# Performance work log

Hardware: AMD Instinct MI355X
Metric: run time of the kernel (lower is better)

The kernel has to match this reference:

```python
import jax, jax.numpy as jnp
import numpy as np
from jax import lax

THETA = 1.0      # neuron['theta']
TAU_SR = 10.0    # neuron['tauSr'] (SRM synaptic time constant)
TAU_RHO = 1.0    # surrogate-gradient width
SCALE_RHO = 1.0  # surrogate-gradient scale
T_SIM = 100      # simulation['tSample']


def srm_kernel(T, dtype=jnp.float32):
    t = jnp.arange(T, dtype=dtype)
    return (t / TAU_SR) * jnp.exp(1.0 - t / TAU_SR)  # eps(0)=0, peak 1 at t=tau


def psp(x, eps):
    """Causal temporal filter along last axis: y[t] = sum_k eps[k] * x[t-k]."""
    shape = x.shape
    T = shape[-1]
    xf = x.reshape(-1, 1, T)
    k = eps[::-1].reshape(1, 1, T)
    y = lax.conv_general_dilated(xf, k, (1,), [(T - 1, 0)],
                                 dimension_numbers=('NCH', 'OIH', 'NCH'))
    return y.reshape(shape)


def spike(u):
    return (u >= THETA).astype(u.dtype)


def conv_t(x, w, pad):
    """Per-timestep 2D conv. x:[B,C,H,W,T], w:[O,I,kh,kw] -> [B,O,H',W',T]."""
    B, C, H, W, T = x.shape
    xt = jnp.moveaxis(x, -1, 1).reshape(B * T, C, H, W)
    y = lax.conv_general_dilated(xt, w, (1, 1), [(pad, pad), (pad, pad)],
                                 dimension_numbers=('NCHW', 'OIHW', 'NCHW'))
    O, Ho, Wo = y.shape[1], y.shape[2], y.shape[3]
    return jnp.moveaxis(y.reshape(B, T, O, Ho, Wo), 1, -1)


def pool2(x):
    """SLAYER pool: 2x2 sum with fixed weight 1.1. x:[B,C,H,W,T]."""
    B, C, H, W, T = x.shape
    xr = x.reshape(B, C, H // 2, 2, W // 2, 2, T)
    return 1.1 * xr.sum(axis=(3, 5))


def dense_t(x, w):
    """x:[B,C,H,W,T] flattened over CHW; w:[O, C*H*W] -> [B,O,T]."""
    B = x.shape[0]
    T = x.shape[-1]
    xf = x.reshape(B, -1, T)
    return jnp.einsum('bit,oi->bot', xf, w)


def setup_inputs() -> dict:
    key = jax.random.key(0)
    k = jax.random.split(key, 6)
    img = jax.random.uniform(k[0], (32, 1, 28, 28), dtype=jnp.float32)
    rand_u = jax.random.uniform(k[1], (32, 1, 28, 28, T_SIM), dtype=jnp.float32)
    w1 = jax.random.normal(k[2], (16, 1, 5, 5), dtype=jnp.float32) * 0.2
    w2 = jax.random.normal(k[3], (32, 16, 5, 5), dtype=jnp.float32) * 0.05
    wf1 = jax.random.normal(k[4], (410, 1568), dtype=jnp.float32) * 0.05
    wf2 = jax.random.normal(k[5], (10, 410), dtype=jnp.float32) * 0.05
    return {"img": img, "rand_u": rand_u, "w1": w1, "w2": w2, "wf1": wf1, "wf2": wf2}


def reference(img, rand_u, w1, w2, wf1, wf2):
    eps = srm_kernel(T_SIM, img.dtype)
    # rate encoding: Bernoulli spikes with p = pixel intensity
    x = (rand_u < img[..., None]).astype(img.dtype)          # [B,1,28,28,T]
    x = spike(psp(conv_t(x, w1, 2), eps))                    # [B,16,28,28,T]
    x = spike(psp(pool2(x), eps))                            # [B,16,14,14,T]
    x = spike(psp(conv_t(x, w2, 2), eps))                    # [B,32,14,14,T]
    x = spike(psp(pool2(x), eps))                            # [B,32,7,7,T]
    x = spike(psp(dense_t(x, wf1), eps))                     # [B,410,T]
    x = spike(psp(jnp.einsum('bit,oi->bot', x, wf2), eps))   # [B,10,T]
    return x
```

## Files before the change

### kernel.cpp

```cpp
#include <hip/hip_runtime.h>


namespace {
constexpr int B = 32, T = 100;
constexpr double A1 = 0.90483741803595957;
constexpr double CE = 0.27182818284590452;
constexpr double SC39 = 549755813888.0;
constexpr double INV39 = 1.0 / 549755813888.0;

constexpr size_t OFF_M1 = 0;
constexpr size_t OFF_M2 = OFF_M1 + (size_t)B * T * 28 * 4;
constexpr size_t OFF_S4 = OFF_M2 + (size_t)B * T * 224 * 4;
constexpr size_t OFF_D5 = OFF_S4 + (size_t)B * T * 1568;
constexpr size_t OFF_S5 = OFF_D5 + (size_t)B * T * 410 * 8;
constexpr size_t OFF_D6 = OFF_S5 + (size_t)B * T * 410;
constexpr size_t OFF_BP = OFF_D6 + (size_t)B * T * 10 * 8;
constexpr size_t OFF_AP = OFF_D5;
}

using i32x4 = __attribute__((ext_vector_type(4))) int;
using i32x16 = __attribute__((ext_vector_type(16))) int;

__global__ void k_encode_pack(const float* __restrict__ img, const float* __restrict__ ru,
                              unsigned int* __restrict__ m1) {
  int i = blockIdx.x * 256 + threadIdx.x;
  if (i >= B * 28 * T) return;
  int t = i % T;
  int y = (i / T) % 28;
  int b = i / (T * 28);
  unsigned int m = 0;
  const float* rb = ru + ((size_t)b * 784 + y * 28) * T + t;
  const float* ib = img + b * 784 + y * 28;
  for (int x = 0; x < 28; x++) {
    m |= (rb[(size_t)x * T] < ib[x]) ? (1u << x) : 0u;
  }
  m1[((size_t)b * T + t) * 28 + y] = m;
}

__global__ __launch_bounds__(256) void k_conv1w(const unsigned int* __restrict__ m1,
                                                const float* __restrict__ w1,
                                                unsigned int* __restrict__ m2) {
  __shared__ double lut2[320 * 2];
  __shared__ unsigned int mrow[2][32];
  int o = blockIdx.x % 16, b = blockIdx.x / 16;
  int tid = threadIdx.x;
  for (int e = tid; e < 320; e += 256) {
    int dy = e / 64, f = e % 64;
    const float* wb = w1 + o * 25 + dy * 5;
    double v0 = 0.0, v1 = 0.0;
#pragma unroll
    for (int dx = 0; dx < 5; dx++) {
      double wv = (double)wb[dx];
      if ((f >> dx) & 1) v0 += wv;
      if ((f >> (dx + 1)) & 1) v1 += wv;
    }
    lut2[e * 2 + 0] = v0;
    lut2[e * 2 + 1] = v1;
  }
  if (tid < 32) {
    mrow[0][tid] = 0;
    mrow[1][tid] = 0;
  }
  int py = tid >> 4, px = tid & 15;
  bool act = (px < 14) && (py < 14);
  int yA = 2 * py, xA = 2 * px;
  double g1[4] = {0, 0, 0, 0}, g2[4] = {0, 0, 0, 0};
  double q1 = 0.0, q2 = 0.0;
  const unsigned int* m1b = m1 + (size_t)b * T * 28;
  if (tid < 28) mrow[0][tid + 2] = m1b[tid] << 2;
  __syncthreads();
  for (int t = 0; t < T; t++) {
    int p = t & 1, np = p ^ 1;
    bool dold = (tid < 28) && (t + 1 < T);
    unsigned int ldv = 0;
    if (dold) ldv = m1b[(t + 1) * 28 + tid] << 2;
    unsigned int poolBit = 0;
    if (act) {
      double sAa = 0, sAb = 0, sBa = 0, sBb = 0;
      const unsigned int* mc = mrow[p];
#pragma unroll
      for (int dy = 0; dy < 5; dy++) {
        unsigned int mA = mc[yA + dy];
        unsigned int mB = mc[yA + 1 + dy];
        const double* eA = lut2 + (dy * 64 + (int)((mA >> xA) & 63u)) * 2;
        const double* eB = lut2 + (dy * 64 + (int)((mB >> xA) & 63u)) * 2;
        sAa += eA[0];
        sAb += eA[1];
        sBa += eB[0];
        sBb += eB[1];
      }
      g1[0] = sAa + A1 * g1[0]; g2[0] = g1[0] + A1 * g2[0];
      g1[1] = sAb + A1 * g1[1]; g2[1] = g1[1] + A1 * g2[1];
      g1[2] = sBa + A1 * g1[2]; g2[2] = g1[2] + A1 * g2[2];
      g1[3] = sBb + A1 * g1[3]; g2[3] = g1[3] + A1 * g2[3];
      int s0 = (CE * (g2[0] - g1[0]) >= 1.0) ? 1 : 0;
      int s1 = (CE * (g2[1] - g1[1]) >= 1.0) ? 1 : 0;
      int s2 = (CE * (g2[2] - g1[2]) >= 1.0) ? 1 : 0;
      int s3 = (CE * (g2[3] - g1[3]) >= 1.0) ? 1 : 0;
      double s = 1.1 * (double)(s0 + s1 + s2 + s3);
      q1 = s + A1 * q1;
      q2 = q1 + A1 * q2;
      poolBit = (CE * (q2 - q1) >= 1.0) ? 1u : 0u;
    }
    unsigned long long bal = __ballot((int)poolBit);
    if (act && px == 0) {
      int lane = tid & 63;
      unsigned int rm = (unsigned int)((bal >> (lane & 48)) & 0x3FFFull);
      m2[((size_t)(b * T + t) * 16 + o) * 14 + py] = rm;
    }
    if (dold) mrow[np][tid + 2] = ldv;
    __syncthreads();
  }
}

__global__ void k_limbs(const float* __restrict__ w2, signed char* __restrict__ AP) {
  int i = blockIdx.x * 256 + threadIdx.x;
  if (i >= 32 * 80 * 8) return;
  int dx = i & 7;
  int g = (i >> 3) % 80;
  int o = i / 640;
  int c = g >> 2, r = g & 3, eh = r >> 1, kh = r & 1;
  int lane = kh * 32 + o, e = eh * 8 + dx;
  int ci = g / 5, dy = g % 5;
  float wv = (dx < 5) ? w2[((o * 16 + ci) * 5 + dy) * 5 + dx] : 0.0f;
  long long m = llrint((double)wv * SC39);
#pragma unroll
  for (int j = 0; j < 5; j++) {
    int d = (int)((m + 128) & 255) - 128;
    AP[(size_t)((j * 20 + c) * 64 + lane) * 16 + e] = (signed char)d;
    m = (m - d) >> 8;
  }
}

__global__ __launch_bounds__(512, 2) void k_conv2v(const unsigned int* __restrict__ m2,
                                                   const signed char* __restrict__ AP,
                                                   unsigned char* __restrict__ s4) {
  __shared__ unsigned int maskW[2][2][192];
  __shared__ unsigned long long part[2][2][32][30];
  int yp = blockIdx.x % 7, b = blockIdx.x / 7;
  int y0 = yp * 2;
  int tid = threadIdx.x;
  int w = tid >> 6, l = tid & 63;
  int tp = w & 1, kq = w >> 1;
  int col = l & 31, kh = l >> 5;
  int x = col % 14;
  unsigned int wmask = (col < 28) ? 31u : 0u;
  int half = (col >= 14) ? 1 : 0;
  const unsigned int* m2b = m2 + (size_t)b * T * 224;

  const i32x4* APv = (const i32x4*)AP;
  i32x4 Af[5][5];
#pragma unroll
  for (int j = 0; j < 5; j++)
#pragma unroll
    for (int q = 0; q < 5; q++)
      Af[j][q] = APv[(size_t)(j * 20 + 5 * kq + q) * 64 + l];

  int stPos[3] = {-1, -1, -1}, stIdx[3] = {-1, -1, -1};
  if (w < 2) {
#pragma unroll
    for (int pass = 0; pass < 3; pass++) {
      if (pass == 2 && l >= 32) continue;
      int e = pass * 64 + l;
      int H = e / 80, g = e % 80;
      int c = g >> 2, eh2 = (g >> 1) & 1, kh2 = g & 1;
      int kq2 = c / 5, q2 = c % 5;
      int ci = g / 5, dy = g % 5;
      int iy = y0 - 2 + H + dy;
      stPos[pass] = H * 96 + kh2 * 48 + kq2 * 12 + q2 * 2 + eh2;
      if (iy >= 0 && iy < 14) stIdx[pass] = ci * 14 + iy;
    }
  }

  int ct = tid - 256;
  bool chainAct = (ct >= 0) && (ct < 224);
  int po = (ct >= 0) ? ct / 7 : 0;
  int pp = (ct >= 0) ? ct % 7 : 0;
  double sg1[4] = {0, 0, 0, 0}, sg2[4] = {0, 0, 0, 0};
  double pq1 = 0.0, pq2 = 0.0;

  {
    unsigned long long* pf = &part[0][0][0][0];
    for (int e = tid; e < 2 * 2 * 32 * 30; e += 512) pf[e] = 0ull;
  }
  if (w < 2) {
#pragma unroll
    for (int pass = 0; pass < 3; pass++) {
      if (stPos[pass] < 0) continue;
      unsigned int v = 0;
      if (stIdx[pass] >= 0) v = m2b[(size_t)w * 224 + stIdx[pass]] << 2;
      maskW[0][w][stPos[pass]] = v;
    }
  }
  __syncthreads();

  for (int grp = 0; grp < 50; grp++) {
    int p = grp & 1, np = p ^ 1;

    unsigned int ld0 = 0, ld1 = 0, ld2 = 0;
    bool doStage = (w < 2) && (grp + 1 < 50);
    if (doStage) {
      size_t tb = (size_t)((grp + 1) * 2 + w) * 224;
      if (stIdx[0] >= 0) ld0 = m2b[tb + stIdx[0]] << 2;
      if (stIdx[1] >= 0) ld1 = m2b[tb + stIdx[1]] << 2;
      if (stIdx[2] >= 0) ld2 = m2b[tb + stIdx[2]] << 2;
    }

    {
      const uint4* mwv = (const uint4*)&maskW[p][tp][0];
      int base4 = half * 24 + kh * 12 + kq * 3;
      uint4 mk0 = mwv[base4 + 0], mk1 = mwv[base4 + 1], mk2 = mwv[base4 + 2];
      i32x16 ac0, ac1, ac2, ac3, ac4;
#pragma unroll
      for (int r = 0; r < 16; r++) { ac0[r] = 0; ac1[r] = 0; ac2[r] = 0; ac3[r] = 0; ac4[r] = 0; }
#pragma unroll
      for (int q = 0; q < 5; q++) {
        unsigned int ra = (q == 0) ? mk0.x : (q == 1) ? mk0.z : (q == 2) ? mk1.x
                         : (q == 3) ? mk1.z : mk2.x;
        unsigned int rb = (q == 0) ? mk0.y : (q == 1) ? mk0.w : (q == 2) ? mk1.y
                         : (q == 3) ? mk1.w : mk2.y;
        unsigned int a5 = (ra >> x) & wmask;
        unsigned int b5 = (rb >> x) & wmask;
        i32x4 bb;
        bb[0] = (int)(((a5 & 15u) * 0x204081u) & 0x01010101u);
        bb[1] = (int)((a5 >> 4) & 1u);
        bb[2] = (int)(((b5 & 15u) * 0x204081u) & 0x01010101u);
        bb[3] = (int)((b5 >> 4) & 1u);
        ac0 = __builtin_amdgcn_mfma_i32_32x32x32_i8(Af[0][q], bb, ac0, 0, 0, 0);
        ac1 = __builtin_amdgcn_mfma_i32_32x32x32_i8(Af[1][q], bb, ac1, 0, 0, 0);
        ac2 = __builtin_amdgcn_mfma_i32_32x32x32_i8(Af[2][q], bb, ac2, 0, 0, 0);
        ac3 = __builtin_amdgcn_mfma_i32_32x32x32_i8(Af[3][q], bb, ac3, 0, 0, 0);
        ac4 = __builtin_amdgcn_mfma_i32_32x32x32_i8(Af[4][q], bb, ac4, 0, 0, 0);
      }
      if (col < 28) {
#pragma unroll
        for (int r = 0; r < 16; r++) {
          int R = (r & 3) + 8 * (r >> 2) + 4 * kh;
          int c01 = ac1[r] * 256 + ac0[r];
          int c23 = ac3[r] * 256 + ac2[r];
          long long S = (long long)ac4[r] * 4294967296LL +
                        (long long)c23 * 65536LL + (long long)c01;
          atomicAdd(&part[p][tp][R][col], (unsigned long long)S);
        }
      }
    }

    if (doStage) {
      if (stPos[0] >= 0) maskW[np][w][stPos[0]] = ld0;
      if (stPos[1] >= 0) maskW[np][w][stPos[1]] = ld1;
      if (stPos[2] >= 0) maskW[np][w][stPos[2]] = ld2;
    }
    __syncthreads();

    if (chainAct) {
#pragma unroll
      for (int g = 0; g < 2; g++) {
        unsigned long long v0 = part[p][g][po][2 * pp];
        unsigned long long v1 = part[p][g][po][2 * pp + 1];
        unsigned long long v2 = part[p][g][po][14 + 2 * pp];
        unsigned long long v3 = part[p][g][po][15 + 2 * pp];
        part[p][g][po][2 * pp] = 0ull;
        part[p][g][po][2 * pp + 1] = 0ull;
        part[p][g][po][14 + 2 * pp] = 0ull;
        part[p][g][po][15 + 2 * pp] = 0ull;
        double c0 = (double)(long long)v0 * INV39;
        double c1 = (double)(long long)v1 * INV39;
        double c2 = (double)(long long)v2 * INV39;
        double c3 = (double)(long long)v3 * INV39;
        sg1[0] = c0 + A1 * sg1[0]; sg2[0] = sg1[0] + A1 * sg2[0];
        sg1[1] = c1 + A1 * sg1[1]; sg2[1] = sg1[1] + A1 * sg2[1];
        sg1[2] = c2 + A1 * sg1[2]; sg2[2] = sg1[2] + A1 * sg2[2];
        sg1[3] = c3 + A1 * sg1[3]; sg2[3] = sg1[3] + A1 * sg2[3];
        int sum = ((CE * (sg2[0] - sg1[0]) >= 1.0) ? 1 : 0)
                + ((CE * (sg2[1] - sg1[1]) >= 1.0) ? 1 : 0)
                + ((CE * (sg2[2] - sg1[2]) >= 1.0) ? 1 : 0)
                + ((CE * (sg2[3] - sg1[3]) >= 1.0) ? 1 : 0);
        double s = 1.1 * (double)sum;
        pq1 = s + A1 * pq1;
        pq2 = pq1 + A1 * pq2;
        s4[(size_t)(b * T + grp * 2 + g) * 1568 + po * 49 + yp * 7 + pp] =
            (CE * (pq2 - pq1) >= 1.0) ? 1 : 0;
      }
    }
  }
}

__global__ void k_limbs2(const float* __restrict__ wf1, signed char* __restrict__ BP) {
  int i = blockIdx.x * 256 + threadIdx.x;
  if (i >= 13 * 5 * 49 * 64) return;
  int lane = i & 63;
  int fi = i >> 6;
  int c = fi % 49;
  int j = (fi / 49) % 5;
  int ot = fi / 245;
  int o = ot * 32 + (lane & 31);
  int kb = 32 * c + (lane >> 5) * 16;
  int wd[4] = {0, 0, 0, 0};
#pragma unroll
  for (int e = 0; e < 16; e++) {
    float wv = (o < 410) ? wf1[(size_t)o * 1568 + kb + e] : 0.0f;
    long long m = llrint((double)wv * SC39);
    int d = 0;
    for (int jj = 0; jj <= j; jj++) {
      d = (int)((m + 128) & 255) - 128;
      m = (m - d) >> 8;
    }
    wd[e >> 2] |= (d & 255) << ((e & 3) * 8);
  }
  i32x4 v;
  v[0] = wd[0]; v[1] = wd[1]; v[2] = wd[2]; v[3] = wd[3];
  *(i32x4*)(BP + (size_t)i * 16) = v;
}

__global__ __launch_bounds__(256) void k_dense1m(const unsigned char* __restrict__ s4,
                                                 const signed char* __restrict__ BP,
                                                 double* __restrict__ d5) {
  int ot = blockIdx.y;
  int w = threadIdx.x >> 6, l = threadIdx.x & 63;
  int col = l & 31, kh = l >> 5;
  int btTile = blockIdx.x * 4 + w;
  const unsigned char* arow = s4 + (size_t)(btTile * 32 + col) * 1568 + kh * 16;
  const i32x4* bpv = (const i32x4*)BP + (size_t)ot * 245 * 64 + l;
  i32x16 acc0, acc1, acc2, acc3, acc4;
#pragma unroll
  for (int r = 0; r < 16; r++) {
    acc0[r] = 0; acc1[r] = 0; acc2[r] = 0; acc3[r] = 0; acc4[r] = 0;
  }
  for (int c = 0; c < 49; c++) {
    i32x4 a = *(const i32x4*)(arow + 32 * c);
    i32x4 b0 = bpv[(0 * 49 + c) * 64];
    i32x4 b1 = bpv[(1 * 49 + c) * 64];
    i32x4 b2 = bpv[(2 * 49 + c) * 64];
    i32x4 b3 = bpv[(3 * 49 + c) * 64];
    i32x4 b4 = bpv[(4 * 49 + c) * 64];
    acc0 = __builtin_amdgcn_mfma_i32_32x32x32_i8(a, b0, acc0, 0, 0, 0);
    acc1 = __builtin_amdgcn_mfma_i32_32x32x32_i8(a, b1, acc1, 0, 0, 0);
    acc2 = __builtin_amdgcn_mfma_i32_32x32x32_i8(a, b2, acc2, 0, 0, 0);
    acc3 = __builtin_amdgcn_mfma_i32_32x32x32_i8(a, b3, acc3, 0, 0, 0);
    acc4 = __builtin_amdgcn_mfma_i32_32x32x32_i8(a, b4, acc4, 0, 0, 0);
  }
  int o = ot * 32 + col;
  if (o < 410) {
#pragma unroll
    for (int r = 0; r < 16; r++) {
      int R = (r & 3) + 8 * (r >> 2) + 4 * kh;
      double v = ((((double)acc4[r] * 256.0 + (double)acc3[r]) * 256.0 +
                   (double)acc2[r]) * 256.0 + (double)acc1[r]) * 256.0 + (double)acc0[r];
      d5[(size_t)(btTile * 32 + R) * 410 + o] = v * INV39;
    }
  }
}

__global__ void k_psp5(const double* __restrict__ d5, unsigned char* __restrict__ s5) {
  int tid = blockIdx.x * 256 + threadIdx.x;
  if (tid >= B * 410) return;
  int o = tid % 410, b = tid / 410;
  double g1 = 0.0, g2 = 0.0;
  for (int t = 0; t < T; t++) {
    double s = d5[(size_t)(b * T + t) * 410 + o];
    g1 = s + A1 * g1;
    g2 = g1 + A1 * g2;
    s5[(size_t)(b * T + t) * 410 + o] = (CE * (g2 - g1) >= 1.0) ? 1 : 0;
  }
}

__global__ void k_dense2(const unsigned char* __restrict__ s5, const float* __restrict__ wf2,
                         double* __restrict__ d6) {
  int tid = blockIdx.x * 256 + threadIdx.x;
  if (tid >= B * T * 10) return;
  int o = tid % 10, bt = tid / 10;
  const unsigned char* sr = s5 + (size_t)bt * 410;
  const float* wr = wf2 + o * 410;
  double s = 0.0;
  for (int i = 0; i < 410; i++) s += (double)wr[i] * (double)sr[i];
  d6[tid] = s;
}

__global__ void k_psp6(const double* __restrict__ d6, float* __restrict__ out) {
  int tid = blockIdx.x * 256 + threadIdx.x;
  if (tid >= B * 10) return;
  int o = tid % 10, b = tid / 10;
  double g1 = 0.0, g2 = 0.0;
  for (int t = 0; t < T; t++) {
    double s = d6[(size_t)(b * T + t) * 10 + o];
    g1 = s + A1 * g1;
    g2 = g1 + A1 * g2;
    out[(size_t)b * 1000 + o * 100 + t] = (CE * (g2 - g1) >= 1.0) ? 1.0f : 0.0f;
  }
}

extern "C" void kernel_launch(void* const* d_in, const int* in_sizes, int n_in,
                              void* d_out, int out_size, void* d_ws, size_t ws_size,
                              hipStream_t stream) {
  const float* img = (const float*)d_in[0];
  const float* ru = (const float*)d_in[1];
  const float* w1 = (const float*)d_in[2];
  const float* w2 = (const float*)d_in[3];
  const float* wf1 = (const float*)d_in[4];
  const float* wf2 = (const float*)d_in[5];

  unsigned char* ws = (unsigned char*)d_ws;
  unsigned int* m1 = (unsigned int*)(ws + OFF_M1);
  unsigned int* m2 = (unsigned int*)(ws + OFF_M2);
  unsigned char* s4 = ws + OFF_S4;
  double* d5 = (double*)(ws + OFF_D5);
  unsigned char* s5 = ws + OFF_S5;
  double* d6 = (double*)(ws + OFF_D6);
  signed char* AP = (signed char*)(ws + OFF_AP);
  signed char* BP = (signed char*)(ws + OFF_BP);
  float* out = (float*)d_out;

  k_encode_pack<<<(B * 28 * T + 255) / 256, 256, 0, stream>>>(img, ru, m1);
  k_limbs<<<(32 * 80 * 8 + 255) / 256, 256, 0, stream>>>(w2, AP);
  k_limbs2<<<(13 * 5 * 49 * 64 + 255) / 256, 256, 0, stream>>>(wf1, BP);
  k_conv1w<<<B * 16, 256, 0, stream>>>(m1, w1, m2);
  k_conv2v<<<B * 7, 512, 0, stream>>>(m2, AP, s4);
  k_dense1m<<<dim3(25, 13), 256, 0, stream>>>(s4, BP, d5);
  k_psp5<<<(B * 410 + 255) / 256, 256, 0, stream>>>(d5, s5);
  k_dense2<<<(B * T * 10 + 255) / 256, 256, 0, stream>>>(s5, wf2, d6);
  k_psp6<<<2, 256, 0, stream>>>(d6, out);
}
```

Before: 345.5 us.

## Move second dense layer onto int8 MFMA with exact limb decomposition

Replaces the scalar fp64 dot-product dense2 kernel with an int8 MFMA kernel. It splits wf2 into five signed 8-bit limbs (a new packing kernel) and pads the s5 rows to 416 so 16-byte loads stay aligned. The PSP kernels now launch in 64-thread blocks, spreading the serial time recurrences over more CUs. The cost is one extra weight-packing launch and padded-column writes, with exactness still resting on the fixed-point limb scheme.

```diff
diff --git a/kernel.cpp b/kernel.cpp
--- a/kernel.cpp
+++ b/kernel.cpp
@@ -13,8 +13,9 @@
 constexpr size_t OFF_S4 = OFF_M2 + (size_t)B * T * 224 * 4;
 constexpr size_t OFF_D5 = OFF_S4 + (size_t)B * T * 1568;
 constexpr size_t OFF_S5 = OFF_D5 + (size_t)B * T * 410 * 8;
-constexpr size_t OFF_D6 = OFF_S5 + (size_t)B * T * 410;
+constexpr size_t OFF_D6 = OFF_S5 + (size_t)B * T * 416;
 constexpr size_t OFF_BP = OFF_D6 + (size_t)B * T * 10 * 8;
+constexpr size_t OFF_BP2 = OFF_BP + (size_t)13 * 5 * 49 * 64 * 16;
 constexpr size_t OFF_AP = OFF_D5;
 }
 
@@ -312,6 +313,33 @@
   *(i32x4*)(BP + (size_t)i * 16) = v;
 }
 
+__global__ void k_limbs3(const float* __restrict__ wf2, signed char* __restrict__ BP2) {
+  int i = blockIdx.x * 256 + threadIdx.x;
+  if (i >= 5 * 13 * 64) return;
+  int lane = i & 63;
+  int fi = i >> 6;
+  int c = fi % 13;
+  int j = fi / 13;
+  int o = lane & 31;
+  int kb = 32 * c + (lane >> 5) * 16;
+  int wd[4] = {0, 0, 0, 0};
+#pragma unroll
+  for (int e = 0; e < 16; e++) {
+    int k = kb + e;
+    float wv = (o < 10 && k < 410) ? wf2[o * 410 + k] : 0.0f;
+    long long m = llrint((double)wv * SC39);
+    int d = 0;
+    for (int jj = 0; jj <= j; jj++) {
+      d = (int)((m + 128) & 255) - 128;
+      m = (m - d) >> 8;
+    }
+    wd[e >> 2] |= (d & 255) << ((e & 3) * 8);
+  }
+  i32x4 v;
+  v[0] = wd[0]; v[1] = wd[1]; v[2] = wd[2]; v[3] = wd[3];
+  *(i32x4*)(BP2 + (size_t)i * 16) = v;
+}
+
 __global__ __launch_bounds__(256) void k_dense1m(const unsigned char* __restrict__ s4,
                                                  const signed char* __restrict__ BP,
                                                  double* __restrict__ d5) {
@@ -352,32 +380,62 @@
 }
 
 __global__ void k_psp5(const double* __restrict__ d5, unsigned char* __restrict__ s5) {
-  int tid = blockIdx.x * 256 + threadIdx.x;
-  if (tid >= B * 410) return;
-  int o = tid % 410, b = tid / 410;
+  int tid = blockIdx.x * 64 + threadIdx.x;
+  if (tid >= B * 416) return;
+  int o = tid % 416, b = tid / 416;
+  if (o >= 410) {
+    for (int t = 0; t < T; t++) s5[(size_t)(b * T + t) * 416 + o] = 0;
+    return;
+  }
   double g1 = 0.0, g2 = 0.0;
   for (int t = 0; t < T; t++) {
     double s = d5[(size_t)(b * T + t) * 410 + o];
     g1 = s + A1 * g1;
     g2 = g1 + A1 * g2;
-    s5[(size_t)(b * T + t) * 410 + o] = (CE * (g2 - g1) >= 1.0) ? 1 : 0;
-  }
-}
-
-__global__ void k_dense2(const unsigned char* __restrict__ s5, const float* __restrict__ wf2,
-                         double* __restrict__ d6) {
-  int tid = blockIdx.x * 256 + threadIdx.x;
-  if (tid >= B * T * 10) return;
-  int o = tid % 10, bt = tid / 10;
-  const unsigned char* sr = s5 + (size_t)bt * 410;
-  const float* wr = wf2 + o * 410;
-  double s = 0.0;
-  for (int i = 0; i < 410; i++) s += (double)wr[i] * (double)sr[i];
-  d6[tid] = s;
+    s5[(size_t)(b * T + t) * 416 + o] = (CE * (g2 - g1) >= 1.0) ? 1 : 0;
+  }
+}
+
+__global__ __launch_bounds__(256) void k_dense2m(const unsigned char* __restrict__ s5,
+                                                 const signed char* __restrict__ BP2,
+                                                 double* __restrict__ d6) {
+  int w = threadIdx.x >> 6, l = threadIdx.x & 63;
+  int col = l & 31, kh = l >> 5;
+  int btTile = blockIdx.x * 4 + w;
+  const unsigned char* arow = s5 + (size_t)(btTile * 32 + col) * 416 + kh * 16;
+  const i32x4* bpv = (const i32x4*)BP2 + l;
+  i32x16 acc0, acc1, acc2, acc3, acc4;
+#pragma unroll
+  for (int r = 0; r < 16; r++) {
+    acc0[r] = 0; acc1[r] = 0; acc2[r] = 0; acc3[r] = 0; acc4[r] = 0;
+  }
+#pragma unroll
+  for (int c = 0; c < 13; c++) {
+    i32x4 a = *(const i32x4*)(arow + 32 * c);
+    i32x4 b0 = bpv[(0 * 13 + c) * 64];
+    i32x4 b1 = bpv[(1 * 13 + c) * 64];
+    i32x4 b2 = bpv[(2 * 13 + c) * 64];
+    i32x4 b3 = bpv[(3 * 13 + c) * 64];
+    i32x4 b4 = bpv[(4 * 13 + c) * 64];
+    acc0 = __builtin_amdgcn_mfma_i32_32x32x32_i8(a, b0, acc0, 0, 0, 0);
+    acc1 = __builtin_amdgcn_mfma_i32_32x32x32_i8(a, b1, acc1, 0, 0, 0);
+    acc2 = __builtin_amdgcn_mfma_i32_32x32x32_i8(a, b2, acc2, 0, 0, 0);
+    acc3 = __builtin_amdgcn_mfma_i32_32x32x32_i8(a, b3, acc3, 0, 0, 0);
+    acc4 = __builtin_amdgcn_mfma_i32_32x32x32_i8(a, b4, acc4, 0, 0, 0);
+  }
+  if (col < 10) {
+#pragma unroll
+    for (int r = 0; r < 16; r++) {
+      int R = (r & 3) + 8 * (r >> 2) + 4 * kh;
+      double v = ((((double)acc4[r] * 256.0 + (double)acc3[r]) * 256.0 +
+                   (double)acc2[r]) * 256.0 + (double)acc1[r]) * 256.0 + (double)acc0[r];
+      d6[(size_t)(btTile * 32 + R) * 10 + col] = v * INV39;
+    }
+  }
 }
 
 __global__ void k_psp6(const double* __restrict__ d6, float* __restrict__ out) {
-  int tid = blockIdx.x * 256 + threadIdx.x;
+  int tid = blockIdx.x * 64 + threadIdx.x;
   if (tid >= B * 10) return;
   int o = tid % 10, b = tid / 10;
   double g1 = 0.0, g2 = 0.0;
@@ -408,15 +466,17 @@
   double* d6 = (double*)(ws + OFF_D6);
   signed char* AP = (signed char*)(ws + OFF_AP);
   signed char* BP = (signed char*)(ws + OFF_BP);
+  signed char* BP2 = (signed char*)(ws + OFF_BP2);
   float* out = (float*)d_out;
 
   k_encode_pack<<<(B * 28 * T + 255) / 256, 256, 0, stream>>>(img, ru, m1);
   k_limbs<<<(32 * 80 * 8 + 255) / 256, 256, 0, stream>>>(w2, AP);
   k_limbs2<<<(13 * 5 * 49 * 64 + 255) / 256, 256, 0, stream>>>(wf1, BP);
+  k_limbs3<<<(5 * 13 * 64 + 255) / 256, 256, 0, stream>>>(wf2, BP2);
   k_conv1w<<<B * 16, 256, 0, stream>>>(m1, w1, m2);
   k_conv2v<<<B * 7, 512, 0, stream>>>(m2, AP, s4);
   k_dense1m<<<dim3(25, 13), 256, 0, stream>>>(s4, BP, d5);
-  k_psp5<<<(B * 410 + 255) / 256, 256, 0, stream>>>(d5, s5);
-  k_dense2<<<(B * T * 10 + 255) / 256, 256, 0, stream>>>(s5, wf2, d6);
-  k_psp6<<<2, 256, 0, stream>>>(d6, out);
-}
+  k_psp5<<<(B * 416 + 63) / 64, 64, 0, stream>>>(d5, s5);
+  k_dense2m<<<25, 256, 0, stream>>>(s5, BP2, d6);
+  k_psp6<<<(B * 10 + 63) / 64, 64, 0, stream>>>(d6, out);
+}
```

Result: slower. 359.9 us (+4.2%).
